# Performance work log

Hardware: AMD Instinct MI355X
Metric: run time of the kernel (lower is better)

Reference implementation:

```python
import jax, jax.numpy as jnp
import numpy as np

EMBED_DIM = 768
NUM_HEADS = 12
NUM_BOND_TYPES = 4
NEG_INF = -1e9


def setup_inputs() -> dict:
    key = jax.random.key(0)
    ks = jax.random.split(key, 8)
    B, N, E = 32, 512, EMBED_DIM
    x = jax.random.normal(ks[0], (B, N, E), dtype=jnp.float32)
    adj = jax.random.randint(ks[1], (B, N, N), 0, 2, dtype=jnp.int32)
    bond = jax.random.randint(ks[2], (B, N, N), 0, NUM_BOND_TYPES + 1, dtype=jnp.int32)
    # nn.Linear(E, 3E): weight (3E, E), bias (3E)
    lim_qkv = 1.0 / np.sqrt(E)
    qkv_w = jax.random.uniform(ks[3], (3 * E, E), minval=-lim_qkv, maxval=lim_qkv, dtype=jnp.float32)
    qkv_b = jax.random.uniform(ks[4], (3 * E,), minval=-lim_qkv, maxval=lim_qkv, dtype=jnp.float32)
    out_w = jax.random.uniform(ks[5], (E, E), minval=-lim_qkv, maxval=lim_qkv, dtype=jnp.float32)
    out_b = jax.random.uniform(ks[6], (E,), minval=-lim_qkv, maxval=lim_qkv, dtype=jnp.float32)
    # nn.Embedding(num_bond_types+1, 1), padding_idx=0 -> row 0 is zero
    bond_table = jax.random.normal(ks[7], (NUM_BOND_TYPES + 1, 1), dtype=jnp.float32)
    bond_table = bond_table.at[0].set(0.0)
    return {"x": x, "adj": adj, "bond": bond, "num_heads": NUM_HEADS,
            "qkv_w": qkv_w, "qkv_b": qkv_b, "out_w": out_w, "out_b": out_b,
            "bond_table": bond_table}


def reference(x, adj, bond, num_heads, qkv_w, qkv_b, out_w, out_b, bond_table):
    B, N, E = x.shape
    hd = E // num_heads
    scale = hd ** -0.5
    # enforce padding_idx=0 semantics
    bond_table = bond_table.at[0].set(0.0)
    qkv = x @ qkv_w.T + qkv_b                      # (B, N, 3E)
    qkv = qkv.reshape(B, N, 3, num_heads, hd).transpose(2, 0, 3, 1, 4)
    q, k, v = qkv[0], qkv[1], qkv[2]               # (B, h, N, hd)
    attn = jnp.einsum('bhnd,bhmd->bhnm', q, k) * scale
    attn = attn + adj.astype(x.dtype)[:, None, :, :]
    bond_bias = bond_table[bond, 0]                # (B, N, N) embedding gather
    attn = attn + bond_bias[:, None, :, :]
    attn = jnp.where(attn == 0, NEG_INF, attn)     # masked_fill(attn == 0)
    attn = jax.nn.softmax(attn, axis=-1)
    out = jnp.einsum('bhnm,bhmd->bhnd', attn, v)   # (B, h, N, hd)
    out = out.transpose(0, 2, 1, 3).reshape(B, N, E)
    return out @ out_w.T + out_b
```

## Files before the change

kernel.cpp:

```cpp
#include <hip/hip_runtime.h>
#include <hip/hip_bf16.h>

typedef __attribute__((ext_vector_type(8))) short short8;
typedef __attribute__((ext_vector_type(8))) unsigned short ushort8;
typedef __attribute__((ext_vector_type(4))) unsigned short ushort4v;
typedef __attribute__((ext_vector_type(4))) float f32x4;
typedef __attribute__((ext_vector_type(4))) unsigned int uint4v;
typedef __attribute__((ext_vector_type(2))) unsigned int uint2v;
typedef __attribute__((ext_vector_type(4))) int int4v;

#define MFMA16(a,b,c) __builtin_amdgcn_mfma_f32_16x16x32_bf16((a),(b),(c),0,0,0)

__device__ __forceinline__ unsigned short f2bf(float f){
    union { float f; unsigned int u; } c; c.f = f;
    unsigned int u = c.u;
    u = (u + 0x7fffu + ((u >> 16) & 1u)) >> 16;
    return (unsigned short)u;
}
__device__ __forceinline__ float bf2f(unsigned short s){
    union { unsigned int u; float f; } c; c.u = ((unsigned int)s) << 16;
    return c.f;
}
__device__ __forceinline__ void split2(float f, unsigned short &h, unsigned short &l){
    h = f2bf(f);
    l = f2bf(f - bf2f(h));
}

__device__ __forceinline__ unsigned int pack_split(float f){
    unsigned int u = __builtin_bit_cast(unsigned int, f);
    float hi = __builtin_bit_cast(float, u & 0xffff0000u);
    unsigned int rem = __builtin_bit_cast(unsigned int, f - hi);
    return __builtin_amdgcn_perm(rem, u, 0x07060302u);
}

__device__ __forceinline__ void unpack8(uint4v u0, uint4v u1, short8& hi, short8& lo){
    uint4v h, l;
    h[0] = __builtin_amdgcn_perm(u0[1], u0[0], 0x05040100u);
    h[1] = __builtin_amdgcn_perm(u0[3], u0[2], 0x05040100u);
    h[2] = __builtin_amdgcn_perm(u1[1], u1[0], 0x05040100u);
    h[3] = __builtin_amdgcn_perm(u1[3], u1[2], 0x05040100u);
    l[0] = __builtin_amdgcn_perm(u0[1], u0[0], 0x07060302u);
    l[1] = __builtin_amdgcn_perm(u0[3], u0[2], 0x07060302u);
    l[2] = __builtin_amdgcn_perm(u1[1], u1[0], 0x07060302u);
    l[3] = __builtin_amdgcn_perm(u1[3], u1[2], 0x07060302u);
    hi = __builtin_bit_cast(short8, h);
    lo = __builtin_bit_cast(short8, l);
}

__global__ void split_kernel(const float* __restrict__ in, unsigned short* __restrict__ h,
                             unsigned short* __restrict__ l, int n){
    int i = blockIdx.x * 256 + threadIdx.x;
    if (i < n){
        unsigned short hh, ll;
        split2(in[i], hh, ll);
        h[i] = hh; l[i] = ll;
    }
}

__global__ void bias_kernel(const int* __restrict__ adj, const int* __restrict__ bond,
                            const float* __restrict__ table, float* __restrict__ biasC, int n4){
    int i = blockIdx.x * 256 + threadIdx.x;
    if (i >= n4) return;
    int4v a  = ((const int4v*)adj)[i];
    int4v bd = ((const int4v*)bond)[i];
    const float t1 = table[1], t2 = table[2], t3 = table[3], t4 = table[4];
    f32x4 o;
    #pragma unroll
    for (int j = 0; j < 4; ++j){
        int bv = bd[j];
        float tb = (bv == 1) ? t1 : (bv == 2) ? t2 : (bv == 3) ? t3 : (bv == 4) ? t4 : 0.0f;
        o[j] = (float)a[j] + tb;
    }
    ((f32x4*)biasC)[i] = o;
}

template<int AMODE, int EMODE>
__global__ __launch_bounds__(256, 2)
void gemm_split(const void* __restrict__ Avoid,
                const unsigned short* __restrict__ Wh, const unsigned short* __restrict__ Wl,
                const float* __restrict__ bias, int N, int K, int NCB, int ROWS_PER_XCD,
                float* __restrict__ C,
                unsigned int* __restrict__ qo, unsigned int* __restrict__ ko,
                unsigned int* __restrict__ vo)
{
    extern __shared__ unsigned short lds[];
    constexpr int LDT = 40;
    constexpr int TSZ = 128 * LDT;
    unsigned short* Ah = lds;
    unsigned short* Al = lds + 2 * TSZ;
    unsigned short* Bh = lds + 4 * TSZ;
    unsigned short* Bl = lds + 6 * TSZ;

    const int lin = blockIdx.x;
    const int xcd = lin & 7, idx = lin >> 3;
    const int rowL = idx / NCB, colT = idx - rowL * NCB;
    const int m0 = (xcd * ROWS_PER_XCD + rowL) * 128;
    const int j0 = colT * 128;

    const int t = threadIdx.x;
    const int l = t & 63, w = t >> 6;
    const int wr = (w >> 1) * 64, wc = (w & 1) * 64;
    const int NT = K >> 5;

    const int a_r = t >> 3, a_c = (t & 7) * 4;
    const int b_r = t >> 2, b_c = (t & 3) * 8;

    f32x4  raf[4];
    uint4v rau[4];
    ushort8 rbh[2], rbl[2];
    f32x4 acc[4][4] = {};

    auto gload = [&](int kt){
        if constexpr (AMODE == 0){
            const float* A = (const float*)Avoid;
            #pragma unroll
            for (int i = 0; i < 4; ++i)
                raf[i] = *(const f32x4*)(A + (size_t)(m0 + i*32 + a_r)*K + kt*32 + a_c);
        } else {
            const unsigned int* A = (const unsigned int*)Avoid;
            #pragma unroll
            for (int i = 0; i < 4; ++i)
                rau[i] = *(const uint4v*)(A + (size_t)(m0 + i*32 + a_r)*K + kt*32 + a_c);
        }
        #pragma unroll
        for (int i = 0; i < 2; ++i){
            int row = i*64 + b_r;
            rbh[i] = *(const ushort8*)(Wh + (size_t)(j0 + row)*K + kt*32 + b_c);
            rbl[i] = *(const ushort8*)(Wl + (size_t)(j0 + row)*K + kt*32 + b_c);
        }
    };
    auto lstore = [&](int buf){
        #pragma unroll
        for (int i = 0; i < 4; ++i){
            int base = buf*TSZ + (i*32 + a_r)*LDT + a_c;
            uint2v hv, lv;
            if constexpr (AMODE == 0){
                unsigned int ub[4], rb[4];
                #pragma unroll
                for (int j = 0; j < 4; ++j){
                    ub[j] = __builtin_bit_cast(unsigned int, raf[i][j]);
                    float hf = __builtin_bit_cast(float, ub[j] & 0xffff0000u);
                    rb[j] = __builtin_bit_cast(unsigned int, raf[i][j] - hf);
                }
                hv[0] = __builtin_amdgcn_perm(ub[1], ub[0], 0x07060302u);
                hv[1] = __builtin_amdgcn_perm(ub[3], ub[2], 0x07060302u);
                lv[0] = __builtin_amdgcn_perm(rb[1], rb[0], 0x07060302u);
                lv[1] = __builtin_amdgcn_perm(rb[3], rb[2], 0x07060302u);
            } else {
                hv[0] = __builtin_amdgcn_perm(rau[i][1], rau[i][0], 0x05040100u);
                hv[1] = __builtin_amdgcn_perm(rau[i][3], rau[i][2], 0x05040100u);
                lv[0] = __builtin_amdgcn_perm(rau[i][1], rau[i][0], 0x07060302u);
                lv[1] = __builtin_amdgcn_perm(rau[i][3], rau[i][2], 0x07060302u);
            }
            *(ushort4v*)(Ah + base) = __builtin_bit_cast(ushort4v, hv);
            *(ushort4v*)(Al + base) = __builtin_bit_cast(ushort4v, lv);
        }
        #pragma unroll
        for (int i = 0; i < 2; ++i){
            int base = buf*TSZ + (i*64 + b_r)*LDT + b_c;
            *(ushort8*)(Bh + base) = rbh[i];
            *(ushort8*)(Bl + base) = rbl[i];
        }
    };

    gload(0);
    lstore(0);
    __syncthreads();
    int cur = 0;

    for (int kt = 0; kt < NT; ++kt){
        if (kt + 1 < NT) gload(kt + 1);

        const int ko_ = (l >> 4) * 8;
        short8 afh[4], afl[4], bfh[4], bfl[4];
        #pragma unroll
        for (int f = 0; f < 4; ++f){
            int arow = wr + f*16 + (l & 15);
            int brow = wc + f*16 + (l & 15);
            afh[f] = *(const short8*)(Ah + cur*TSZ + arow*LDT + ko_);
            afl[f] = *(const short8*)(Al + cur*TSZ + arow*LDT + ko_);
            bfh[f] = *(const short8*)(Bh + cur*TSZ + brow*LDT + ko_);
            bfl[f] = *(const short8*)(Bl + cur*TSZ + brow*LDT + ko_);
        }
        __builtin_amdgcn_s_setprio(1);
        #pragma unroll
        for (int fr = 0; fr < 4; ++fr)
            #pragma unroll
            for (int fc = 0; fc < 4; ++fc){
                acc[fr][fc] = MFMA16(afh[fr], bfh[fc], acc[fr][fc]);
                acc[fr][fc] = MFMA16(afh[fr], bfl[fc], acc[fr][fc]);
                acc[fr][fc] = MFMA16(afl[fr], bfh[fc], acc[fr][fc]);
            }
        __builtin_amdgcn_s_setprio(0);

        if (kt + 1 < NT) lstore(cur ^ 1);
        __syncthreads();
        cur ^= 1;
    }

    #pragma unroll
    for (int fr = 0; fr < 4; ++fr){
        #pragma unroll
        for (int fc = 0; fc < 4; ++fc){
            #pragma unroll
            for (int r = 0; r < 4; ++r){
                int m = m0 + wr + fr*16 + ((l >> 4) << 2) + r;
                int j = j0 + wc + fc*16 + (l & 15);
                float val = acc[fr][fc][r] + bias[j];
                if constexpr (EMODE == 0){
                    C[(size_t)m * N + j] = val;
                } else {
                    int sec = j / 768;
                    int off = j - sec * 768;
                    int head = off >> 6, d = off & 63;
                    int bb = m >> 9, n = m & 511;
                    unsigned int packed = pack_split(val);
                    if (sec == 2) {
                        vo[(((size_t)bb * 12 + head) * 64 + d) * 512 + n] = packed;
                    } else {
                        unsigned int* dst = (sec == 0) ? qo : ko;
                        dst[(((size_t)bb * 12 + head) * 512 + n) * 64 + d] = packed;
                    }
                }
            }
        }
    }
}

__global__ __launch_bounds__(256, 3)
void attn_kernel(const unsigned int* __restrict__ qb,
                 const unsigned int* __restrict__ kb,
                 const unsigned int* __restrict__ vtb,
                 const float* __restrict__ biasC,
                 unsigned int* __restrict__ o)
{
    __shared__ unsigned int Kt[64 * 64];
    __shared__ unsigned int Vt[64 * 64];
    __shared__ unsigned int Pt[4][16 * 68];

    const int lin = blockIdx.x;
    const int xcd = lin & 7, m_ = lin >> 3;
    const int bgrp = m_ / 96, r_ = m_ - bgrp * 96;
    const int b = (bgrp << 3) | xcd;
    const int h = r_ >> 3, qt = r_ & 7;
    const int bh = b * 12 + h, q0 = qt * 64;

    const int t = threadIdx.x, l = t & 63, w = t >> 6;
    const int c = l & 15, g = l >> 4;

    const unsigned int* qp  = qb  + (size_t)bh * 512 * 64;
    const unsigned int* kp  = kb  + (size_t)bh * 512 * 64;
    const unsigned int* vtp = vtb + (size_t)bh * 64 * 512;

    short8 qh[2], ql[2];
    {
        int qrow = q0 + w*16 + c;
        #pragma unroll
        for (int ks = 0; ks < 2; ++ks){
            const unsigned int* p = qp + (size_t)qrow * 64 + ks*32 + g*8;
            uint4v u0 = *(const uint4v*)p;
            uint4v u1 = *(const uint4v*)(p + 4);
            unpack8(u0, u1, qh[ks], ql[ks]);
        }
    }

    f32x4 O[4] = {};
    float mrow[4] = {-3e38f, -3e38f, -3e38f, -3e38f};
    float lrow[4] = {0.f, 0.f, 0.f, 0.f};

    const int srow = t >> 2;
    const int scol = (t & 3) * 16;
    const int ssw  = (srow & 7) << 4;

    auto rdfrag = [&](const unsigned int* base, int row, int colb, short8& hi, short8& lo){
        int sw = (row & 7) << 4;
        const char* p = (const char*)base + row*256;
        uint4v u0 = *(const uint4v*)(p + ((colb     ) ^ sw));
        uint4v u1 = *(const uint4v*)(p + ((colb + 16) ^ sw));
        unpack8(u0, u1, hi, lo);
    };

    for (int kt = 0; kt < 8; ++kt){
        {
            const unsigned int* kg = kp  + (size_t)(kt*64 + srow) * 64 + scol;
            const unsigned int* vg = vtp + (size_t)srow * 512 + kt*64 + scol;
            #pragma unroll
            for (int i = 0; i < 4; ++i){
                uint4v a  = *(const uint4v*)(kg + 4*i);
                uint4v bx = *(const uint4v*)(vg + 4*i);
                int cb = (scol + 4*i) * 4;
                *(uint4v*)((char*)Kt + srow*256 + (cb ^ ssw)) = a;
                *(uint4v*)((char*)Vt + srow*256 + (cb ^ ssw)) = bx;
            }
        }
        __syncthreads();

        float bia[4][4];
        #pragma unroll
        for (int fc = 0; fc < 4; ++fc){
            #pragma unroll
            for (int r = 0; r < 4; ++r){
                int rr = q0 + w*16 + g*4 + r;
                int cc = kt*64 + fc*16 + c;
                bia[fc][r] = biasC[((size_t)b * 512 + rr) * 512 + cc];
            }
        }

        f32x4 S[4] = {};
        #pragma unroll
        for (int fc = 0; fc < 4; ++fc){
            short8 kbh0, kbl0, kbh1, kbl1;
            rdfrag(Kt, fc*16 + c,       g*32, kbh0, kbl0);
            rdfrag(Kt, fc*16 + c, 128 + g*32, kbh1, kbl1);
            __builtin_amdgcn_s_setprio(1);
            S[fc] = MFMA16(qh[0], kbh0, S[fc]);
            S[fc] = MFMA16(qh[0], kbl0, S[fc]);
            S[fc] = MFMA16(ql[0], kbh0, S[fc]);
            S[fc] = MFMA16(qh[1], kbh1, S[fc]);
            S[fc] = MFMA16(qh[1], kbl1, S[fc]);
            S[fc] = MFMA16(ql[1], kbh1, S[fc]);
            __builtin_amdgcn_s_setprio(0);
        }

        float sv[4][4];
        #pragma unroll
        for (int fc = 0; fc < 4; ++fc){
            #pragma unroll
            for (int r = 0; r < 4; ++r){
                float val = fmaf(S[fc][r], 0.125f, bia[fc][r]);
                if (val == 0.0f) val = -1e9f;
                sv[fc][r] = val;
            }
        }

        float pvreg[4][4];
        #pragma unroll
        for (int r = 0; r < 4; ++r){
            float mt = fmaxf(fmaxf(sv[0][r], sv[1][r]), fmaxf(sv[2][r], sv[3][r]));
            #pragma unroll
            for (int off = 1; off < 16; off <<= 1)
                mt = fmaxf(mt, __shfl_xor(mt, off, 16));
            float mn = fmaxf(mrow[r], mt);
            float corr = __expf(mrow[r] - mn);
            float rs = 0.0f;
            #pragma unroll
            for (int fc = 0; fc < 4; ++fc){
                float p = __expf(sv[fc][r] - mn);
                pvreg[fc][r] = p;
                rs += p;
            }
            #pragma unroll
            for (int off = 1; off < 16; off <<= 1)
                rs += __shfl_xor(rs, off, 16);
            lrow[r] = lrow[r] * corr + rs;
            mrow[r] = mn;
            #pragma unroll
            for (int hf = 0; hf < 4; ++hf)
                O[hf][r] *= corr;
        }

        #pragma unroll
        for (int fc = 0; fc < 4; ++fc){
            #pragma unroll
            for (int r = 0; r < 4; ++r){
                Pt[w][(g*4 + r)*68 + fc*16 + c] = pack_split(pvreg[fc][r]);
            }
        }

        #pragma unroll
        for (int ks = 0; ks < 2; ++ks){
            const unsigned int* pp = &Pt[w][c*68 + ks*32 + g*8];
            uint4v pu0 = *(const uint4v*)pp;
            uint4v pu1 = *(const uint4v*)(pp + 4);
            short8 pah, pal;
            unpack8(pu0, pu1, pah, pal);
            #pragma unroll
            for (int hf = 0; hf < 4; ++hf){
                short8 vbh, vbl;
                rdfrag(Vt, hf*16 + c, ks*128 + g*32, vbh, vbl);
                __builtin_amdgcn_s_setprio(1);
                O[hf] = MFMA16(pah, vbh, O[hf]);
                O[hf] = MFMA16(pah, vbl, O[hf]);
                O[hf] = MFMA16(pal, vbh, O[hf]);
                __builtin_amdgcn_s_setprio(0);
            }
        }
        __syncthreads();
    }

    #pragma unroll
    for (int r = 0; r < 4; ++r){
        float inv = 1.0f / lrow[r];
        int rr = q0 + w*16 + g*4 + r;
        #pragma unroll
        for (int hf = 0; hf < 4; ++hf){
            int col = h*64 + hf*16 + c;
            o[((size_t)b * 512 + rr) * 768 + col] = pack_split(O[hf][r] * inv);
        }
    }
}

extern "C" void kernel_launch(void* const* d_in, const int* in_sizes, int n_in,
                              void* d_out, int out_size, void* d_ws, size_t ws_size,
                              hipStream_t stream)
{
    const float* x     = (const float*)d_in[0];
    const int*   adj   = (const int*)d_in[1];
    const int*   bond  = (const int*)d_in[2];
    const float* qkv_w = (const float*)d_in[4];
    const float* qkv_b = (const float*)d_in[5];
    const float* out_w = (const float*)d_in[6];
    const float* out_b = (const float*)d_in[7];
    const float* btab  = (const float*)d_in[8];
    float* out = (float*)d_out;

    const int QKV_ELEMS = 32 * 12 * 512 * 64;
    unsigned int* q  = (unsigned int*)d_ws;
    unsigned int* k  = q + QKV_ELEMS;
    unsigned int* vt = k + QKV_ELEMS;
    unsigned int* o  = vt + QKV_ELEMS;
    unsigned short* woh = (unsigned short*)(o + QKV_ELEMS);
    unsigned short* wol = woh + 768 * 768;
    unsigned short* wqh = wol + 768 * 768;
    unsigned short* wql = wqh + 2304 * 768;
    float* biasC = (float*)(wqh);

    dim3 blk(256);
    split_kernel<<<dim3((2304*768 + 255)/256), blk, 0, stream>>>(qkv_w, wqh, wql, 2304*768);
    split_kernel<<<dim3((768*768 + 255)/256),  blk, 0, stream>>>(out_w, woh, wol, 768*768);

    gemm_split<0,1><<<dim3(2304), blk, 81920, stream>>>(
        x, wqh, wql, qkv_b, 2304, 768, 18, 16, nullptr, q, k, vt);

    bias_kernel<<<dim3(8192), blk, 0, stream>>>(adj, bond, btab, biasC, (32*512*512)/4);

    attn_kernel<<<dim3(3072), blk, 0, stream>>>(q, k, vt, biasC, o);

    gemm_split<1,0><<<dim3(768), blk, 81920, stream>>>(
        o, woh, wol, out_b, 768, 768, 6, 16, out, nullptr, nullptr, nullptr);
}
```

Baseline: 478.0 us.

## Pre-pack GEMM operands into swizzled tile images loaded via direct-to-LDS copies

Both GEMMs now read operands from pre-packed tile images: x and the weights are split into hi/lo bf16 pairs by packing kernels. The attention kernel writes its output straight into the same swizzled 128x32 tile layout. The GEMM copies each tile with global_load_lds into an XOR-swizzled LDS buffer, which removes the register staging and in-kernel conversion and cuts LDS use so the occupancy hint rises from 2 to 3. In exchange it adds an extra pass over x, loses the double-buffered prefetch, and makes the loop load-then-sync single-buffered, which may expose memory latency.

```diff
diff --git a/kernel.cpp b/kernel.cpp
--- a/kernel.cpp
+++ b/kernel.cpp
@@ -2,14 +2,15 @@
 #include <hip/hip_bf16.h>
 
 typedef __attribute__((ext_vector_type(8))) short short8;
-typedef __attribute__((ext_vector_type(8))) unsigned short ushort8;
-typedef __attribute__((ext_vector_type(4))) unsigned short ushort4v;
 typedef __attribute__((ext_vector_type(4))) float f32x4;
 typedef __attribute__((ext_vector_type(4))) unsigned int uint4v;
-typedef __attribute__((ext_vector_type(2))) unsigned int uint2v;
 typedef __attribute__((ext_vector_type(4))) int int4v;
 
 #define MFMA16(a,b,c) __builtin_amdgcn_mfma_f32_16x16x32_bf16((a),(b),(c),0,0,0)
+
+#define GLOAD_LDS16(g, l) \
+    __builtin_amdgcn_global_load_lds((const __attribute__((address_space(1))) void*)(g), \
+                                     (__attribute__((address_space(3))) void*)(l), 16, 0, 0)
 
 __device__ __forceinline__ unsigned short f2bf(float f){
     union { float f; unsigned int u; } c; c.f = f;
@@ -20,10 +21,6 @@
 __device__ __forceinline__ float bf2f(unsigned short s){
     union { unsigned int u; float f; } c; c.u = ((unsigned int)s) << 16;
     return c.f;
-}
-__device__ __forceinline__ void split2(float f, unsigned short &h, unsigned short &l){
-    h = f2bf(f);
-    l = f2bf(f - bf2f(h));
 }
 
 __device__ __forceinline__ unsigned int pack_split(float f){
@@ -47,14 +44,33 @@
     lo = __builtin_bit_cast(short8, l);
 }
 
-__global__ void split_kernel(const float* __restrict__ in, unsigned short* __restrict__ h,
-                             unsigned short* __restrict__ l, int n){
-    int i = blockIdx.x * 256 + threadIdx.x;
-    if (i < n){
-        unsigned short hh, ll;
-        split2(in[i], hh, ll);
-        h[i] = hh; l[i] = ll;
-    }
+__global__ void pack_x_kernel(const float* __restrict__ x, unsigned int* __restrict__ img){
+    int tid = blockIdx.x * 256 + threadIdx.x;
+    int m = tid / 192, k4 = (tid - m*192) * 4;
+    f32x4 v = *(const f32x4*)(x + (size_t)m*768 + k4);
+    uint4v p;
+    #pragma unroll
+    for (int j = 0; j < 4; ++j) p[j] = pack_split(v[j]);
+    int mt = m >> 7, row = m & 127, kt = k4 >> 5, u = k4 & 31;
+    size_t off = ((size_t)(mt*24 + kt))*16384 + row*128 + (size_t)((u*4) ^ ((row&7)<<4));
+    *(uint4v*)((char*)img + off) = p;
+}
+
+__global__ void pack_w_kernel(const float* __restrict__ wsrc, unsigned int* __restrict__ img, int total){
+    int tid = blockIdx.x * 256 + threadIdx.x;
+    if (tid >= total) return;
+    int n = tid / 192, k4 = (tid - n*192) * 4;
+    f32x4 v = *(const f32x4*)(wsrc + (size_t)n*768 + k4);
+    uint4v p;
+    #pragma unroll
+    for (int j = 0; j < 4; ++j){
+        unsigned short hh = f2bf(v[j]);
+        unsigned short ll = f2bf(v[j] - bf2f(hh));
+        p[j] = (unsigned int)hh | ((unsigned int)ll << 16);
+    }
+    int jt = n >> 7, row = n & 127, kt = k4 >> 5, u = k4 & 31;
+    size_t off = ((size_t)(jt*24 + kt))*16384 + row*128 + (size_t)((u*4) ^ ((row&7)<<4));
+    *(uint4v*)((char*)img + off) = p;
 }
 
 __global__ void bias_kernel(const int* __restrict__ adj, const int* __restrict__ bond,
@@ -74,128 +90,73 @@
     ((f32x4*)biasC)[i] = o;
 }
 
-template<int AMODE, int EMODE>
-__global__ __launch_bounds__(256, 2)
-void gemm_split(const void* __restrict__ Avoid,
-                const unsigned short* __restrict__ Wh, const unsigned short* __restrict__ Wl,
-                const float* __restrict__ bias, int N, int K, int NCB, int ROWS_PER_XCD,
-                float* __restrict__ C,
-                unsigned int* __restrict__ qo, unsigned int* __restrict__ ko,
-                unsigned int* __restrict__ vo)
+template<int EMODE>
+__global__ __launch_bounds__(256, 3)
+void gemm_img(const unsigned int* __restrict__ Aimg, const unsigned int* __restrict__ Bimg,
+              const float* __restrict__ bias, int NT, int RPX,
+              float* __restrict__ C, int N,
+              unsigned int* __restrict__ qo, unsigned int* __restrict__ ko,
+              unsigned int* __restrict__ vo)
 {
-    extern __shared__ unsigned short lds[];
-    constexpr int LDT = 40;
-    constexpr int TSZ = 128 * LDT;
-    unsigned short* Ah = lds;
-    unsigned short* Al = lds + 2 * TSZ;
-    unsigned short* Bh = lds + 4 * TSZ;
-    unsigned short* Bl = lds + 6 * TSZ;
+    __shared__ unsigned int lds[8192];
 
     const int lin = blockIdx.x;
     const int xcd = lin & 7, idx = lin >> 3;
-    const int rowL = idx / NCB, colT = idx - rowL * NCB;
-    const int m0 = (xcd * ROWS_PER_XCD + rowL) * 128;
-    const int j0 = colT * 128;
-
-    const int t = threadIdx.x;
-    const int l = t & 63, w = t >> 6;
-    const int wr = (w >> 1) * 64, wc = (w & 1) * 64;
-    const int NT = K >> 5;
-
-    const int a_r = t >> 3, a_c = (t & 7) * 4;
-    const int b_r = t >> 2, b_c = (t & 3) * 8;
-
-    f32x4  raf[4];
-    uint4v rau[4];
-    ushort8 rbh[2], rbl[2];
+    const int grp  = idx / (RPX * 6);
+    const int rem  = idx - grp * (RPX * 6);
+    const int rowL = rem / 6, c6 = rem - rowL * 6;
+    const int colT = grp * 6 + c6;
+    const int mt = xcd * RPX + rowL;
+    const int m0 = mt << 7, j0 = colT << 7;
+
+    const int t = threadIdx.x, l = t & 63, w = t >> 6;
+    const int c = l & 15, g = l >> 4;
+    const int wr = (w >> 1) * 64, wc2 = (w & 1) * 64;
+
+    const unsigned int* Ablk = Aimg + (size_t)mt   * NT * 4096;
+    const unsigned int* Bblk = Bimg + (size_t)colT * NT * 4096;
+
     f32x4 acc[4][4] = {};
 
-    auto gload = [&](int kt){
-        if constexpr (AMODE == 0){
-            const float* A = (const float*)Avoid;
-            #pragma unroll
-            for (int i = 0; i < 4; ++i)
-                raf[i] = *(const f32x4*)(A + (size_t)(m0 + i*32 + a_r)*K + kt*32 + a_c);
-        } else {
-            const unsigned int* A = (const unsigned int*)Avoid;
-            #pragma unroll
-            for (int i = 0; i < 4; ++i)
-                rau[i] = *(const uint4v*)(A + (size_t)(m0 + i*32 + a_r)*K + kt*32 + a_c);
-        }
-        #pragma unroll
-        for (int i = 0; i < 2; ++i){
-            int row = i*64 + b_r;
-            rbh[i] = *(const ushort8*)(Wh + (size_t)(j0 + row)*K + kt*32 + b_c);
-            rbl[i] = *(const ushort8*)(Wl + (size_t)(j0 + row)*K + kt*32 + b_c);
-        }
-    };
-    auto lstore = [&](int buf){
+    for (int kt = 0; kt < NT; ++kt){
+        const unsigned int* As = Ablk + kt*4096 + t*4;
+        const unsigned int* Bs = Bblk + kt*4096 + t*4;
+        unsigned int* Ad = lds + t*4;
+        unsigned int* Bd = lds + 4096 + t*4;
         #pragma unroll
         for (int i = 0; i < 4; ++i){
-            int base = buf*TSZ + (i*32 + a_r)*LDT + a_c;
-            uint2v hv, lv;
-            if constexpr (AMODE == 0){
-                unsigned int ub[4], rb[4];
-                #pragma unroll
-                for (int j = 0; j < 4; ++j){
-                    ub[j] = __builtin_bit_cast(unsigned int, raf[i][j]);
-                    float hf = __builtin_bit_cast(float, ub[j] & 0xffff0000u);
-                    rb[j] = __builtin_bit_cast(unsigned int, raf[i][j] - hf);
-                }
-                hv[0] = __builtin_amdgcn_perm(ub[1], ub[0], 0x07060302u);
-                hv[1] = __builtin_amdgcn_perm(ub[3], ub[2], 0x07060302u);
-                lv[0] = __builtin_amdgcn_perm(rb[1], rb[0], 0x07060302u);
-                lv[1] = __builtin_amdgcn_perm(rb[3], rb[2], 0x07060302u);
-            } else {
-                hv[0] = __builtin_amdgcn_perm(rau[i][1], rau[i][0], 0x05040100u);
-                hv[1] = __builtin_amdgcn_perm(rau[i][3], rau[i][2], 0x05040100u);
-                lv[0] = __builtin_amdgcn_perm(rau[i][1], rau[i][0], 0x07060302u);
-                lv[1] = __builtin_amdgcn_perm(rau[i][3], rau[i][2], 0x07060302u);
-            }
-            *(ushort4v*)(Ah + base) = __builtin_bit_cast(ushort4v, hv);
-            *(ushort4v*)(Al + base) = __builtin_bit_cast(ushort4v, lv);
-        }
-        #pragma unroll
-        for (int i = 0; i < 2; ++i){
-            int base = buf*TSZ + (i*64 + b_r)*LDT + b_c;
-            *(ushort8*)(Bh + base) = rbh[i];
-            *(ushort8*)(Bl + base) = rbl[i];
-        }
-    };
-
-    gload(0);
-    lstore(0);
-    __syncthreads();
-    int cur = 0;
-
-    for (int kt = 0; kt < NT; ++kt){
-        if (kt + 1 < NT) gload(kt + 1);
-
-        const int ko_ = (l >> 4) * 8;
-        short8 afh[4], afl[4], bfh[4], bfl[4];
-        #pragma unroll
-        for (int f = 0; f < 4; ++f){
-            int arow = wr + f*16 + (l & 15);
-            int brow = wc + f*16 + (l & 15);
-            afh[f] = *(const short8*)(Ah + cur*TSZ + arow*LDT + ko_);
-            afl[f] = *(const short8*)(Al + cur*TSZ + arow*LDT + ko_);
-            bfh[f] = *(const short8*)(Bh + cur*TSZ + brow*LDT + ko_);
-            bfl[f] = *(const short8*)(Bl + cur*TSZ + brow*LDT + ko_);
-        }
-        __builtin_amdgcn_s_setprio(1);
-        #pragma unroll
-        for (int fr = 0; fr < 4; ++fr)
+            GLOAD_LDS16(As + i*1024, Ad + i*1024);
+            GLOAD_LDS16(Bs + i*1024, Bd + i*1024);
+        }
+        __syncthreads();
+
+        short8 bh[4], bl[4];
+        #pragma unroll
+        for (int fc = 0; fc < 4; ++fc){
+            int row = wc2 + fc*16 + c;
+            int sw = (row & 7) << 4;
+            const char* p = (const char*)(lds + 4096) + row*128;
+            uint4v u0 = *(const uint4v*)(p + ((g*32     ) ^ sw));
+            uint4v u1 = *(const uint4v*)(p + ((g*32 + 16) ^ sw));
+            unpack8(u0, u1, bh[fc], bl[fc]);
+        }
+        #pragma unroll
+        for (int fr = 0; fr < 4; ++fr){
+            int row = wr + fr*16 + c;
+            int sw = (row & 7) << 4;
+            const char* p = (const char*)lds + row*128;
+            uint4v u0 = *(const uint4v*)(p + ((g*32     ) ^ sw));
+            uint4v u1 = *(const uint4v*)(p + ((g*32 + 16) ^ sw));
+            short8 ah, al;
+            unpack8(u0, u1, ah, al);
             #pragma unroll
             for (int fc = 0; fc < 4; ++fc){
-                acc[fr][fc] = MFMA16(afh[fr], bfh[fc], acc[fr][fc]);
-                acc[fr][fc] = MFMA16(afh[fr], bfl[fc], acc[fr][fc]);
-                acc[fr][fc] = MFMA16(afl[fr], bfh[fc], acc[fr][fc]);
-            }
-        __builtin_amdgcn_s_setprio(0);
-
-        if (kt + 1 < NT) lstore(cur ^ 1);
+                acc[fr][fc] = MFMA16(ah, bh[fc], acc[fr][fc]);
+                acc[fr][fc] = MFMA16(ah, bl[fc], acc[fr][fc]);
+                acc[fr][fc] = MFMA16(al, bh[fc], acc[fr][fc]);
+            }
+        }
         __syncthreads();
-        cur ^= 1;
     }
 
     #pragma unroll
@@ -204,8 +165,8 @@
         for (int fc = 0; fc < 4; ++fc){
             #pragma unroll
             for (int r = 0; r < 4; ++r){
-                int m = m0 + wr + fr*16 + ((l >> 4) << 2) + r;
-                int j = j0 + wc + fc*16 + (l & 15);
+                int m = m0 + wr + fr*16 + g*4 + r;
+                int j = j0 + wc2 + fc*16 + c;
                 float val = acc[fr][fc][r] + bias[j];
                 if constexpr (EMODE == 0){
                     C[(size_t)m * N + j] = val;
@@ -232,7 +193,7 @@
                  const unsigned int* __restrict__ kb,
                  const unsigned int* __restrict__ vtb,
                  const float* __restrict__ biasC,
-                 unsigned int* __restrict__ o)
+                 unsigned int* __restrict__ oimg)
 {
     __shared__ unsigned int Kt[64 * 64];
     __shared__ unsigned int Vt[64 * 64];
@@ -391,11 +352,16 @@
     #pragma unroll
     for (int r = 0; r < 4; ++r){
         float inv = 1.0f / lrow[r];
-        int rr = q0 + w*16 + g*4 + r;
+        int m = b*512 + q0 + w*16 + g*4 + r;
+        int mt = m >> 7, mrow2 = m & 127;
+        int swz = (mrow2 & 7) << 4;
+        size_t rowbase = ((size_t)mt*24)*16384 + (size_t)mrow2*128;
         #pragma unroll
         for (int hf = 0; hf < 4; ++hf){
-            int col = h*64 + hf*16 + c;
-            o[((size_t)b * 512 + rr) * 768 + col] = pack_split(O[hf][r] * inv);
+            int e = h*64 + hf*16 + c;
+            int kt2 = e >> 5, u = e & 31;
+            size_t off = rowbase + (size_t)kt2*16384 + (size_t)((u*4) ^ swz);
+            *(unsigned int*)((char*)oimg + off) = pack_split(O[hf][r] * inv);
         }
     }
 }
@@ -414,28 +380,28 @@
     const float* btab  = (const float*)d_in[8];
     float* out = (float*)d_out;
 
-    const int QKV_ELEMS = 32 * 12 * 512 * 64;
-    unsigned int* q  = (unsigned int*)d_ws;
-    unsigned int* k  = q + QKV_ELEMS;
-    unsigned int* vt = k + QKV_ELEMS;
-    unsigned int* o  = vt + QKV_ELEMS;
-    unsigned short* woh = (unsigned short*)(o + QKV_ELEMS);
-    unsigned short* wol = woh + 768 * 768;
-    unsigned short* wqh = wol + 768 * 768;
-    unsigned short* wql = wqh + 2304 * 768;
-    float* biasC = (float*)(wqh);
+    const size_t QKV = 12582912;
+    unsigned int* q   = (unsigned int*)d_ws;
+    unsigned int* k   = q  + QKV;
+    unsigned int* vt  = k  + QKV;
+    unsigned int* r1  = vt + QKV;
+    unsigned int* w2i = r1 + QKV;
+    unsigned int* r2  = w2i + 589824;
+    unsigned int* w1i = r2;
+    float* biasC      = (float*)r2;
 
     dim3 blk(256);
-    split_kernel<<<dim3((2304*768 + 255)/256), blk, 0, stream>>>(qkv_w, wqh, wql, 2304*768);
-    split_kernel<<<dim3((768*768 + 255)/256),  blk, 0, stream>>>(out_w, woh, wol, 768*768);
-
-    gemm_split<0,1><<<dim3(2304), blk, 81920, stream>>>(
-        x, wqh, wql, qkv_b, 2304, 768, 18, 16, nullptr, q, k, vt);
+    pack_w_kernel<<<dim3(1728), blk, 0, stream>>>(qkv_w, w1i, 2304*192);
+    pack_w_kernel<<<dim3(576),  blk, 0, stream>>>(out_w, w2i, 768*192);
+    pack_x_kernel<<<dim3(12288), blk, 0, stream>>>(x, r1);
+
+    gemm_img<1><<<dim3(2304), blk, 0, stream>>>(r1, w1i, qkv_b, 24, 16,
+                                                nullptr, 2304, q, k, vt);
 
     bias_kernel<<<dim3(8192), blk, 0, stream>>>(adj, bond, btab, biasC, (32*512*512)/4);
 
-    attn_kernel<<<dim3(3072), blk, 0, stream>>>(q, k, vt, biasC, o);
-
-    gemm_split<1,0><<<dim3(768), blk, 81920, stream>>>(
-        o, woh, wol, out_b, 768, 768, 6, 16, out, nullptr, nullptr, nullptr);
-}
+    attn_kernel<<<dim3(3072), blk, 0, stream>>>(q, k, vt, biasC, r1);
+
+    gemm_img<0><<<dim3(768), blk, 0, stream>>>(r1, w2i, out_b, 24, 16,
+                                               out, 768, nullptr, nullptr, nullptr);
+}
```

Measured after the change: 437.1 us. 1.09x faster.
